# Kernel optimization log

Measured on AMD Instinct MI355X. Metric: run time of the kernel, lower is better.

## Reference

```python
import jax, jax.numpy as jnp
import numpy as np

INPUT_SIZE = 64
HIDDEN = 256
OUTPUT_SIZE = 64
NUM_LAYERS = 2
MAX_LENGTH = 512
BATCH = 1024


def setup_inputs() -> dict:
    key = jax.random.key(0)
    ks = jax.random.split(key, 14)
    s = 1.0 / np.sqrt(HIDDEN)  # torch LSTM/Linear init scale
    f32 = jnp.float32
    inp = {
        "batch_size": BATCH,
        "h0": jax.random.normal(ks[0], (NUM_LAYERS, BATCH, HIDDEN), f32),
        "c0": jax.random.normal(ks[1], (NUM_LAYERS, BATCH, HIDDEN), f32),
        "Wih0": jax.random.uniform(ks[2], (4 * HIDDEN, INPUT_SIZE), f32, -s, s),
        "Whh0": jax.random.uniform(ks[3], (4 * HIDDEN, HIDDEN), f32, -s, s),
        "bih0": jax.random.uniform(ks[4], (4 * HIDDEN,), f32, -s, s),
        "bhh0": jax.random.uniform(ks[5], (4 * HIDDEN,), f32, -s, s),
        "Wih1": jax.random.uniform(ks[6], (4 * HIDDEN, HIDDEN), f32, -s, s),
        "Whh1": jax.random.uniform(ks[7], (4 * HIDDEN, HIDDEN), f32, -s, s),
        "bih1": jax.random.uniform(ks[8], (4 * HIDDEN,), f32, -s, s),
        "bhh1": jax.random.uniform(ks[9], (4 * HIDDEN,), f32, -s, s),
        "Wfc": jax.random.uniform(ks[10], (OUTPUT_SIZE, HIDDEN), f32, -s, s),
        "bfc": jax.random.uniform(ks[11], (OUTPUT_SIZE,), f32, -s, s),
    }
    return inp


def _lstm_cell(x, h, c, Wih, Whh, bih, bhh):
    # torch gate order: input, forget, cell(g), output
    gates = x @ Wih.T + h @ Whh.T + bih + bhh  # [B, 4H]
    i, f, g, o = jnp.split(gates, 4, axis=-1)
    c_new = jax.nn.sigmoid(f) * c + jax.nn.sigmoid(i) * jnp.tanh(g)
    h_new = jax.nn.sigmoid(o) * jnp.tanh(c_new)
    return h_new, c_new


def reference(batch_size, h0, c0, Wih0, Whh0, bih0, bhh0, Wih1, Whh1, bih1, bhh1, Wfc, bfc):
    # initial decoder input: zeros with the (-3)rd feature set to 1 (SOS token)
    x0 = jnp.zeros((batch_size, INPUT_SIZE), h0.dtype).at[:, -3].set(1.0)

    def step(carry, _):
        x, h, c = carry  # h, c: [num_layers, B, H]
        h0_new, c0_new = _lstm_cell(x, h[0], c[0], Wih0, Whh0, bih0, bhh0)
        h1_new, c1_new = _lstm_cell(h0_new, h[1], c[1], Wih1, Whh1, bih1, bhh1)
        pred = h1_new @ Wfc.T + bfc  # [B, output_size]
        acts = jax.nn.log_softmax(pred[:, : OUTPUT_SIZE - 1], axis=-1)
        dur = jax.nn.sigmoid(pred[:, OUTPUT_SIZE - 1 :])
        out = jnp.concatenate([acts, dur], axis=-1)
        h_new = jnp.stack([h0_new, h1_new])
        c_new = jnp.stack([c0_new, c1_new])
        return (out, h_new, c_new), out

    (x_f, h_f, c_f), outs = jax.lax.scan(step, (x0, h0, c0), None, length=MAX_LENGTH)
    outputs = jnp.transpose(outs, (1, 0, 2))  # [B, max_length, output_size]
    return outputs, h_f, c_f
```

## Files before the change

### kernel.cpp

```cpp
#include <hip/hip_runtime.h>
#include <stdint.h>
#include <stddef.h>


#define NGROUP 16
#define GWG    16
#define NTHR   512
#define TSTEPS 512

typedef _Float16 half8 __attribute__((ext_vector_type(8)));
typedef float    f32x4 __attribute__((ext_vector_type(4)));

#define OUT_ELEMS   33554432
#define HF_ELEMS    524288
#define HBUF_ELEMS  16384
#define GROUP_WS_BYTES 65536
#define WS_HBUF_OFF 4096
#define WS_NEEDED   (WS_HBUF_OFF + NGROUP * GROUP_WS_BYTES)

__device__ __forceinline__ float sigm(float x)   { return 1.0f / (1.0f + __expf(-x)); }
__device__ __forceinline__ float tanh_f(float x) { return 1.0f - 2.0f / (__expf(2.0f * x) + 1.0f); }

__device__ __forceinline__ void group_barrier(int* ctr, int* phase, int zz) {
  __syncthreads();
  if (threadIdx.x == 0) {
    __hip_atomic_fetch_add(ctr, 1, __ATOMIC_RELEASE, __HIP_MEMORY_SCOPE_WORKGROUP);
    const int target = GWG * (++(*phase));
    while (__hip_atomic_fetch_add(ctr, zz, __ATOMIC_RELAXED, __HIP_MEMORY_SCOPE_WORKGROUP) < target)
      __builtin_amdgcn_s_sleep(1);
    asm volatile("buffer_inv sc0" ::: "memory");
  }
  __syncthreads();
}

__device__ __forceinline__ half8 ld_frag(const _Float16* buf, int idx16) {
  return *(const half8*)(buf + (size_t)idx16 * 8);
}

__device__ __forceinline__ void stage32k8(const void* src, void* lds_dst, int tid) {
  const int wv = tid >> 6;
  const int ln = tid & 63;
  const char* s = (const char*)src + ln * 16;
  char* d = (char*)lds_dst;
  #pragma unroll
  for (int i = 0; i < 4; ++i) {
    const int off = (i * 8 + wv) * 1024;
    __builtin_amdgcn_global_load_lds(
        (const __attribute__((address_space(1))) void*)(s + off),
        (__attribute__((address_space(3))) void*)(d + off),
        16, 0, 0);
  }
}

__global__ __launch_bounds__(NTHR, 2)
void decoder_kernel(const float* __restrict__ h0in, const float* __restrict__ c0in,
                    const float* __restrict__ Wih0, const float* __restrict__ Whh0,
                    const float* __restrict__ bih0, const float* __restrict__ bhh0,
                    const float* __restrict__ Wih1, const float* __restrict__ Whh1,
                    const float* __restrict__ bih1, const float* __restrict__ bhh1,
                    const float* __restrict__ Wfc,  const float* __restrict__ bfc,
                    float* __restrict__ out, char* __restrict__ ws)
{
  const int tid  = threadIdx.x;
  const int lane = tid & 63;
  const int wave = tid >> 6;
  const int mi   = wave >> 2;
  const int nj   = wave & 3;
  const int q    = lane >> 4;
  const int u    = lane & 15;
  const int em   = tid >> 3;
  const int eu2  = (tid & 7) * 2;

  int zz;
  asm volatile("s_mov_b32 %0, 0" : "=s"(zz));

  __shared__ int s_gw[2];
  if (tid == 0) {
    uint32_t xcc;
    asm volatile("s_getreg_b32 %0, hwreg(HW_REG_XCC_ID)" : "=s"(xcc));
    xcc &= 7;
    const int slot = atomicAdd((int*)(ws + 2048) + (size_t)xcc * 32, 1);
    s_gw[0] = (int)xcc * 2 + (slot >> 4);
    s_gw[1] = slot & 15;
  }
  __syncthreads();
  const int g = s_gw[0];
  const int w = s_gw[1];

  int* ctr = (int*)(ws + (size_t)g * 128);
  _Float16* h0b = (_Float16*)(ws + WS_HBUF_OFF + (size_t)g * GROUP_WS_BYTES);
  _Float16* h1b = h0b + HBUF_ELEMS;

  __shared__ __align__(16) _Float16 sb0[HBUF_ELEMS];
  __shared__ __align__(16) _Float16 sb1[HBUF_ELEMS];
  __shared__ __align__(16) _Float16 wfcs[32 * 65 * 8];
  __shared__ __align__(16) _Float16 xbuf[64 * 72];
  __shared__ __align__(16) float    exch[4 * 64 * 17];
  __shared__ __align__(16) float    predbuf[64 * 68];

  half8 bL0[10]; half8 bL1[16];
  float biasL0, biasL1, biasFC;
  {
    const int row = nj * 256 + w * 16 + u;
    biasL0 = bih0[row] + bhh0[row];
    biasL1 = bih1[row] + bhh1[row];
    #pragma unroll
    for (int kt = 0; kt < 10; ++kt) {
      const int k0 = kt * 32 + q * 8;
      const float* src = (kt < 2) ? (Wih0 + (size_t)row * 64 + k0)
                                  : (Whh0 + (size_t)row * 256 + (k0 - 64));
      half8 v;
      #pragma unroll
      for (int j = 0; j < 8; ++j) v[j] = (_Float16)src[j];
      bL0[kt] = v;
    }
    #pragma unroll
    for (int kt = 0; kt < 16; ++kt) {
      const int k0 = kt * 32 + q * 8;
      const float* src = (kt < 8) ? (Wih1 + (size_t)row * 256 + k0)
                                  : (Whh1 + (size_t)row * 256 + (k0 - 256));
      half8 v;
      #pragma unroll
      for (int j = 0; j < 8; ++j) v[j] = (_Float16)src[j];
      bL1[kt] = v;
    }
    biasFC = bfc[nj * 16 + u];
  }
  for (int i = tid; i < 2048; i += NTHR) {
    const int rowF = i & 63;
    const int c    = i >> 6;
    const float* s = Wfc + (size_t)rowF * 256 + c * 8;
    half8 v;
    #pragma unroll
    for (int j = 0; j < 8; ++j) v[j] = (_Float16)s[j];
    *(half8*)(wfcs + (size_t)(c * 65 + rowF) * 8) = v;
  }

  float c0st[2], c1st[2], h0sv[2], h1sv[2];
  #pragma unroll
  for (int e = 0; e < 2; ++e) {
    const size_t idx = (size_t)(g * 64 + em) * 256 + w * 16 + eu2 + e;
    c0st[e] = c0in[idx];
    c1st[e] = c0in[262144 + idx];
    h0sv[e] = 0.0f; h1sv[e] = 0.0f;
  }
  {
    const int cg2 = w * 2 + (eu2 >> 3);
    const uint32_t slot = (uint32_t)(cg2 * 64 + em) * 4 + ((eu2 & 7) >> 1);
    #pragma unroll
    for (int l = 0; l < 2; ++l) {
      const float* s = h0in + (size_t)l * 262144 + (size_t)(g * 64 + em) * 256 + w * 16 + eu2;
      union { _Float16 h[2]; uint32_t u32; } pk;
      pk.h[0] = (_Float16)s[0]; pk.h[1] = (_Float16)s[1];
      ((uint32_t*)(l ? h1b : h0b))[slot] = pk.u32;
    }
  }
  for (int i = tid; i < 64 * 64; i += NTHR) {
    const int row = i >> 6, col = i & 63;
    xbuf[row * 72 + col] = (col == 61) ? (_Float16)1.0f : (_Float16)0.0f;
  }

  int phase = 0;
  group_barrier(ctr, &phase, zz);

  stage32k8(h0b, sb0, tid);
  stage32k8(h1b, sb1, tid);
  __syncthreads();

  for (int t = 0; t < TSTEPS; ++t) {
    {
      f32x4 acc[2];
      #pragma unroll
      for (int mt = 0; mt < 2; ++mt) {
        f32x4 v; v[0] = biasL0; v[1] = biasL0; v[2] = biasL0; v[3] = biasL0;
        acc[mt] = v;
      }
      #pragma unroll
      for (int kt = 0; kt < 10; ++kt) {
        half8 a[2];
        #pragma unroll
        for (int mt = 0; mt < 2; ++mt) {
          const int m = mi * 32 + mt * 16 + u;
          if (kt < 2) a[mt] = *(const half8*)(xbuf + m * 72 + kt * 32 + q * 8);
          else        a[mt] = *(const half8*)(sb0 + (size_t)((kt * 4 - 8 + q) * 64 + m) * 8);
        }
        #pragma unroll
        for (int mt = 0; mt < 2; ++mt)
          acc[mt] = __builtin_amdgcn_mfma_f32_16x16x32_f16(a[mt], bL0[kt], acc[mt], 0, 0, 0);
      }
      #pragma unroll
      for (int mt = 0; mt < 2; ++mt)
        #pragma unroll
        for (int r = 0; r < 4; ++r)
          exch[(nj * 64 + mi * 32 + mt * 16 + q * 4 + r) * 17 + u] = acc[mt][r];
    }
    __syncthreads();
    {
      float hv[2];
      #pragma unroll
      for (int e = 0; e < 2; ++e) {
        const int ec = eu2 + e;
        const float iv = exch[(0 * 64 + em) * 17 + ec];
        const float fv = exch[(1 * 64 + em) * 17 + ec];
        const float gv = exch[(2 * 64 + em) * 17 + ec];
        const float ov = exch[(3 * 64 + em) * 17 + ec];
        const float cn = sigm(fv) * c0st[e] + sigm(iv) * tanh_f(gv);
        c0st[e] = cn;
        const float hh = sigm(ov) * tanh_f(cn);
        h0sv[e] = hh; hv[e] = hh;
      }
      union { _Float16 h[2]; uint32_t u32; } pk;
      pk.h[0] = (_Float16)hv[0]; pk.h[1] = (_Float16)hv[1];
      ((uint32_t*)h0b)[(uint32_t)((w * 2 + (eu2 >> 3)) * 64 + em) * 4 + ((eu2 & 7) >> 1)] = pk.u32;
    }
    group_barrier(ctr, &phase, zz);

    stage32k8(h0b, sb0, tid);

    {
      f32x4 acc[2];
      #pragma unroll
      for (int mt = 0; mt < 2; ++mt) {
        f32x4 v; v[0] = biasL1; v[1] = biasL1; v[2] = biasL1; v[3] = biasL1;
        acc[mt] = v;
      }
      #pragma unroll
      for (int kt = 8; kt < 16; ++kt) {
        half8 a[2];
        #pragma unroll
        for (int mt = 0; mt < 2; ++mt) {
          const int m = mi * 32 + mt * 16 + u;
          a[mt] = *(const half8*)(sb1 + (size_t)(((kt - 8) * 4 + q) * 64 + m) * 8);
        }
        #pragma unroll
        for (int mt = 0; mt < 2; ++mt)
          acc[mt] = __builtin_amdgcn_mfma_f32_16x16x32_f16(a[mt], bL1[kt], acc[mt], 0, 0, 0);
      }
      __syncthreads();
      #pragma unroll
      for (int kt = 0; kt < 8; ++kt) {
        half8 a[2];
        #pragma unroll
        for (int mt = 0; mt < 2; ++mt) {
          const int m = mi * 32 + mt * 16 + u;
          a[mt] = *(const half8*)(sb0 + (size_t)((kt * 4 + q) * 64 + m) * 8);
        }
        #pragma unroll
        for (int mt = 0; mt < 2; ++mt)
          acc[mt] = __builtin_amdgcn_mfma_f32_16x16x32_f16(a[mt], bL1[kt], acc[mt], 0, 0, 0);
      }
      #pragma unroll
      for (int mt = 0; mt < 2; ++mt)
        #pragma unroll
        for (int r = 0; r < 4; ++r)
          exch[(nj * 64 + mi * 32 + mt * 16 + q * 4 + r) * 17 + u] = acc[mt][r];
    }
    __syncthreads();
    {
      float hv[2];
      #pragma unroll
      for (int e = 0; e < 2; ++e) {
        const int ec = eu2 + e;
        const float iv = exch[(0 * 64 + em) * 17 + ec];
        const float fv = exch[(1 * 64 + em) * 17 + ec];
        const float gv = exch[(2 * 64 + em) * 17 + ec];
        const float ov = exch[(3 * 64 + em) * 17 + ec];
        const float cn = sigm(fv) * c1st[e] + sigm(iv) * tanh_f(gv);
        c1st[e] = cn;
        const float hh = sigm(ov) * tanh_f(cn);
        h1sv[e] = hh; hv[e] = hh;
      }
      union { _Float16 h[2]; uint32_t u32; } pk;
      pk.h[0] = (_Float16)hv[0]; pk.h[1] = (_Float16)hv[1];
      ((uint32_t*)h1b)[(uint32_t)((w * 2 + (eu2 >> 3)) * 64 + em) * 4 + ((eu2 & 7) >> 1)] = pk.u32;
    }
    group_barrier(ctr, &phase, zz);

    stage32k8(h1b, sb1, tid);

    {
      f32x4 accF[2];
      #pragma unroll
      for (int mt = 0; mt < 2; ++mt) {
        f32x4 v; v[0] = biasFC; v[1] = biasFC; v[2] = biasFC; v[3] = biasFC;
        accF[mt] = v;
      }
      #pragma unroll
      for (int kt = 0; kt < 8; ++kt) {
        const half8 b = *(const half8*)(wfcs + (size_t)((kt * 4 + q) * 65 + nj * 16 + u) * 8);
        half8 a[2];
        #pragma unroll
        for (int mt = 0; mt < 2; ++mt)
          a[mt] = ld_frag(h1b, (kt * 4 + q) * 64 + (mi * 32 + mt * 16 + u));
        #pragma unroll
        for (int mt = 0; mt < 2; ++mt)
          accF[mt] = __builtin_amdgcn_mfma_f32_16x16x32_f16(a[mt], b, accF[mt], 0, 0, 0);
      }
      #pragma unroll
      for (int mt = 0; mt < 2; ++mt)
        #pragma unroll
        for (int r = 0; r < 4; ++r)
          predbuf[(mi * 32 + mt * 16 + q * 4 + r) * 68 + nj * 16 + u] = accF[mt][r];
    }
    __syncthreads();
    {
      const int row = tid >> 3;
      const int cg  = tid & 7;
      const float* pr = predbuf + row * 68 + cg * 8;
      float p[8];
      #pragma unroll
      for (int j = 0; j < 8; ++j) p[j] = pr[j];
      float mx = -3.0e38f;
      #pragma unroll
      for (int j = 0; j < 8; ++j)
        if (!(cg == 7 && j == 7)) mx = fmaxf(mx, p[j]);
      mx = fmaxf(mx, __shfl_xor(mx, 1));
      mx = fmaxf(mx, __shfl_xor(mx, 2));
      mx = fmaxf(mx, __shfl_xor(mx, 4));
      float sm = 0.0f;
      #pragma unroll
      for (int j = 0; j < 8; ++j)
        if (!(cg == 7 && j == 7)) sm += __expf(p[j] - mx);
      sm += __shfl_xor(sm, 1);
      sm += __shfl_xor(sm, 2);
      sm += __shfl_xor(sm, 4);
      const float lz = mx + __logf(sm);
      float o[8];
      #pragma unroll
      for (int j = 0; j < 8; ++j) o[j] = p[j] - lz;
      if (cg == 7) o[7] = sigm(p[7]);
      _Float16* xw = xbuf + row * 72 + cg * 8;
      #pragma unroll
      for (int j = 0; j < 8; ++j) xw[j] = (_Float16)o[j];
      if ((row >> 2) == w) {
        const int ch = g * 64 + row;
        float* dst = out + ((size_t)ch * TSTEPS + t) * 64 + cg * 8;
        #pragma unroll
        for (int j = 0; j < 8; ++j) dst[j] = o[j];
      }
    }
    __syncthreads();
  }

  {
    float* hfp = out + OUT_ELEMS;
    float* cfp = out + OUT_ELEMS + HF_ELEMS;
    #pragma unroll
    for (int e = 0; e < 2; ++e) {
      const size_t idx = (size_t)(g * 64 + em) * 256 + w * 16 + eu2 + e;
      hfp[idx]          = h0sv[e];
      hfp[262144 + idx] = h1sv[e];
      cfp[idx]          = c0st[e];
      cfp[262144 + idx] = c1st[e];
    }
  }
}

extern "C" void kernel_launch(void* const* d_in, const int* in_sizes, int n_in,
                              void* d_out, int out_size, void* d_ws, size_t ws_size,
                              hipStream_t stream) {
  (void)in_sizes; (void)n_in; (void)out_size;
  if (ws_size < (size_t)WS_NEEDED) return;

  const float* h0   = (const float*)d_in[1];
  const float* c0   = (const float*)d_in[2];
  const float* Wih0 = (const float*)d_in[3];
  const float* Whh0 = (const float*)d_in[4];
  const float* bih0 = (const float*)d_in[5];
  const float* bhh0 = (const float*)d_in[6];
  const float* Wih1 = (const float*)d_in[7];
  const float* Whh1 = (const float*)d_in[8];
  const float* bih1 = (const float*)d_in[9];
  const float* bhh1 = (const float*)d_in[10];
  const float* Wfc  = (const float*)d_in[11];
  const float* bfc  = (const float*)d_in[12];
  float* outp = (float*)d_out;
  char*  wsp  = (char*)d_ws;

  hipMemsetAsync(d_ws, 0, WS_HBUF_OFF, stream);

  void* args[] = { &h0, &c0, &Wih0, &Whh0, &bih0, &bhh0, &Wih1, &Whh1,
                   &bih1, &bhh1, &Wfc, &bfc, &outp, &wsp };
  hipError_t e = hipLaunchCooperativeKernel((const void*)decoder_kernel,
                                            dim3(NGROUP * GWG), dim3(NTHR),
                                            args, 0u, stream);
  if (e != hipSuccess) {
    decoder_kernel<<<dim3(NGROUP * GWG), dim3(NTHR), 0, stream>>>(
        h0, c0, Wih0, Whh0, bih0, bhh0, Wih1, Whh1, bih1, bhh1, Wfc, bfc, outp, wsp);
  }
}
```

Before: 3.340 ms.

## Split batch into 32 groups of 32 rows to double workgroup count

```diff
diff --git a/kernel.cpp b/kernel.cpp
--- a/kernel.cpp
+++ b/kernel.cpp
@@ -3,7 +3,7 @@
 #include <stddef.h>
 
 
-#define NGROUP 16
+#define NGROUP 32
 #define GWG    16
 #define NTHR   512
 #define TSTEPS 512
@@ -13,9 +13,10 @@
 
 #define OUT_ELEMS   33554432
 #define HF_ELEMS    524288
-#define HBUF_ELEMS  16384
-#define GROUP_WS_BYTES 65536
-#define WS_HBUF_OFF 4096
+#define HBUF_ELEMS  8192
+#define GROUP_WS_BYTES 32768
+#define WS_SLOT_OFF 4096
+#define WS_HBUF_OFF 8192
 #define WS_NEEDED   (WS_HBUF_OFF + NGROUP * GROUP_WS_BYTES)
 
 __device__ __forceinline__ float sigm(float x)   { return 1.0f / (1.0f + __expf(-x)); }
@@ -37,13 +38,13 @@
   return *(const half8*)(buf + (size_t)idx16 * 8);
 }
 
-__device__ __forceinline__ void stage32k8(const void* src, void* lds_dst, int tid) {
+__device__ __forceinline__ void stage16k8(const void* src, void* lds_dst, int tid) {
   const int wv = tid >> 6;
   const int ln = tid & 63;
   const char* s = (const char*)src + ln * 16;
   char* d = (char*)lds_dst;
   #pragma unroll
-  for (int i = 0; i < 4; ++i) {
+  for (int i = 0; i < 2; ++i) {
     const int off = (i * 8 + wv) * 1024;
     __builtin_amdgcn_global_load_lds(
         (const __attribute__((address_space(1))) void*)(s + off),
@@ -52,7 +53,7 @@
   }
 }
 
-__global__ __launch_bounds__(NTHR, 2)
+__global__ __launch_bounds__(NTHR, 4)
 void decoder_kernel(const float* __restrict__ h0in, const float* __restrict__ c0in,
                     const float* __restrict__ Wih0, const float* __restrict__ Whh0,
                     const float* __restrict__ bih0, const float* __restrict__ bhh0,
@@ -68,8 +69,8 @@
   const int nj   = wave & 3;
   const int q    = lane >> 4;
   const int u    = lane & 15;
-  const int em   = tid >> 3;
-  const int eu2  = (tid & 7) * 2;
+  const int em   = tid >> 4;
+  const int eu   = tid & 15;
 
   int zz;
   asm volatile("s_mov_b32 %0, 0" : "=s"(zz));
@@ -79,8 +80,8 @@
     uint32_t xcc;
     asm volatile("s_getreg_b32 %0, hwreg(HW_REG_XCC_ID)" : "=s"(xcc));
     xcc &= 7;
-    const int slot = atomicAdd((int*)(ws + 2048) + (size_t)xcc * 32, 1);
-    s_gw[0] = (int)xcc * 2 + (slot >> 4);
+    const int slot = atomicAdd((int*)(ws + WS_SLOT_OFF) + (size_t)xcc * 32, 1);
+    s_gw[0] = (int)xcc * 4 + (slot >> 4);
     s_gw[1] = slot & 15;
   }
   __syncthreads();
@@ -94,9 +95,10 @@
   __shared__ __align__(16) _Float16 sb0[HBUF_ELEMS];
   __shared__ __align__(16) _Float16 sb1[HBUF_ELEMS];
   __shared__ __align__(16) _Float16 wfcs[32 * 65 * 8];
-  __shared__ __align__(16) _Float16 xbuf[64 * 72];
-  __shared__ __align__(16) float    exch[4 * 64 * 17];
-  __shared__ __align__(16) float    predbuf[64 * 68];
+  __shared__ __align__(16) _Float16 xbuf[32 * 72];
+  __shared__ __align__(16) float    xpbuf[2176];
+  float* exch    = xpbuf;
+  float* predbuf = xpbuf;
 
   half8 bL0[10]; half8 bL1[16];
   float biasL0, biasL1, biasFC;
@@ -136,26 +138,26 @@
     *(half8*)(wfcs + (size_t)(c * 65 + rowF) * 8) = v;
   }
 
-  float c0st[2], c1st[2], h0sv[2], h1sv[2];
-  #pragma unroll
-  for (int e = 0; e < 2; ++e) {
-    const size_t idx = (size_t)(g * 64 + em) * 256 + w * 16 + eu2 + e;
-    c0st[e] = c0in[idx];
-    c1st[e] = c0in[262144 + idx];
-    h0sv[e] = 0.0f; h1sv[e] = 0.0f;
-  }
+  float c0st, c1st, h0sv = 0.0f, h1sv = 0.0f;
   {
-    const int cg2 = w * 2 + (eu2 >> 3);
-    const uint32_t slot = (uint32_t)(cg2 * 64 + em) * 4 + ((eu2 & 7) >> 1);
+    const size_t idx = (size_t)(g * 32 + em) * 256 + w * 16 + eu;
+    c0st = c0in[idx];
+    c1st = c0in[262144 + idx];
+  }
+  if (tid < 64) {
+    const int m  = tid & 31;
+    const int cc = tid >> 5;
+    const int c  = w * 2 + cc;
     #pragma unroll
     for (int l = 0; l < 2; ++l) {
-      const float* s = h0in + (size_t)l * 262144 + (size_t)(g * 64 + em) * 256 + w * 16 + eu2;
-      union { _Float16 h[2]; uint32_t u32; } pk;
-      pk.h[0] = (_Float16)s[0]; pk.h[1] = (_Float16)s[1];
-      ((uint32_t*)(l ? h1b : h0b))[slot] = pk.u32;
-    }
-  }
-  for (int i = tid; i < 64 * 64; i += NTHR) {
+      const float* s = h0in + (size_t)l * 262144 + (size_t)(g * 32 + m) * 256 + c * 8;
+      half8 pk;
+      #pragma unroll
+      for (int j = 0; j < 8; ++j) pk[j] = (_Float16)s[j];
+      *(half8*)((l ? h1b : h0b) + (size_t)(c * 32 + m) * 8) = pk;
+    }
+  }
+  for (int i = tid; i < 32 * 64; i += NTHR) {
     const int row = i >> 6, col = i & 63;
     xbuf[row * 72 + col] = (col == 61) ? (_Float16)1.0f : (_Float16)0.0f;
   }
@@ -163,180 +165,138 @@
   int phase = 0;
   group_barrier(ctr, &phase, zz);
 
-  stage32k8(h0b, sb0, tid);
-  stage32k8(h1b, sb1, tid);
+  stage16k8(h0b, sb0, tid);
+  stage16k8(h1b, sb1, tid);
   __syncthreads();
 
   for (int t = 0; t < TSTEPS; ++t) {
     {
-      f32x4 acc[2];
-      #pragma unroll
-      for (int mt = 0; mt < 2; ++mt) {
-        f32x4 v; v[0] = biasL0; v[1] = biasL0; v[2] = biasL0; v[3] = biasL0;
-        acc[mt] = v;
-      }
+      f32x4 acc;
+      acc[0] = biasL0; acc[1] = biasL0; acc[2] = biasL0; acc[3] = biasL0;
+      const int m_ = mi * 16 + u;
       #pragma unroll
       for (int kt = 0; kt < 10; ++kt) {
-        half8 a[2];
-        #pragma unroll
-        for (int mt = 0; mt < 2; ++mt) {
-          const int m = mi * 32 + mt * 16 + u;
-          if (kt < 2) a[mt] = *(const half8*)(xbuf + m * 72 + kt * 32 + q * 8);
-          else        a[mt] = *(const half8*)(sb0 + (size_t)((kt * 4 - 8 + q) * 64 + m) * 8);
-        }
-        #pragma unroll
-        for (int mt = 0; mt < 2; ++mt)
-          acc[mt] = __builtin_amdgcn_mfma_f32_16x16x32_f16(a[mt], bL0[kt], acc[mt], 0, 0, 0);
-      }
-      #pragma unroll
-      for (int mt = 0; mt < 2; ++mt)
-        #pragma unroll
-        for (int r = 0; r < 4; ++r)
-          exch[(nj * 64 + mi * 32 + mt * 16 + q * 4 + r) * 17 + u] = acc[mt][r];
+        half8 a;
+        if (kt < 2) a = *(const half8*)(xbuf + m_ * 72 + kt * 32 + q * 8);
+        else        a = *(const half8*)(sb0 + (size_t)((kt * 4 - 8 + q) * 32 + m_) * 8);
+        acc = __builtin_amdgcn_mfma_f32_16x16x32_f16(a, bL0[kt], acc, 0, 0, 0);
+      }
+      #pragma unroll
+      for (int r = 0; r < 4; ++r)
+        exch[(nj * 32 + mi * 16 + q * 4 + r) * 17 + u] = acc[r];
     }
     __syncthreads();
     {
-      float hv[2];
-      #pragma unroll
-      for (int e = 0; e < 2; ++e) {
-        const int ec = eu2 + e;
-        const float iv = exch[(0 * 64 + em) * 17 + ec];
-        const float fv = exch[(1 * 64 + em) * 17 + ec];
-        const float gv = exch[(2 * 64 + em) * 17 + ec];
-        const float ov = exch[(3 * 64 + em) * 17 + ec];
-        const float cn = sigm(fv) * c0st[e] + sigm(iv) * tanh_f(gv);
-        c0st[e] = cn;
-        const float hh = sigm(ov) * tanh_f(cn);
-        h0sv[e] = hh; hv[e] = hh;
-      }
-      union { _Float16 h[2]; uint32_t u32; } pk;
-      pk.h[0] = (_Float16)hv[0]; pk.h[1] = (_Float16)hv[1];
-      ((uint32_t*)h0b)[(uint32_t)((w * 2 + (eu2 >> 3)) * 64 + em) * 4 + ((eu2 & 7) >> 1)] = pk.u32;
+      const float iv = exch[(0 * 32 + em) * 17 + eu];
+      const float fv = exch[(1 * 32 + em) * 17 + eu];
+      const float gv = exch[(2 * 32 + em) * 17 + eu];
+      const float ov = exch[(3 * 32 + em) * 17 + eu];
+      const float cn = sigm(fv) * c0st + sigm(iv) * tanh_f(gv);
+      c0st = cn;
+      const float hh = sigm(ov) * tanh_f(cn);
+      h0sv = hh;
+      const float other = __shfl_xor(hh, 1);
+      if (!(eu & 1)) {
+        union { _Float16 h[2]; uint32_t u32; } pk;
+        pk.h[0] = (_Float16)hh; pk.h[1] = (_Float16)other;
+        ((uint32_t*)h0b)[(uint32_t)((w * 2 + (eu >> 3)) * 32 + em) * 4 + ((eu & 7) >> 1)] = pk.u32;
+      }
     }
     group_barrier(ctr, &phase, zz);
 
-    stage32k8(h0b, sb0, tid);
-
-    {
-      f32x4 acc[2];
-      #pragma unroll
-      for (int mt = 0; mt < 2; ++mt) {
-        f32x4 v; v[0] = biasL1; v[1] = biasL1; v[2] = biasL1; v[3] = biasL1;
-        acc[mt] = v;
-      }
+    stage16k8(h0b, sb0, tid);
+
+    {
+      f32x4 acc;
+      acc[0] = biasL1; acc[1] = biasL1; acc[2] = biasL1; acc[3] = biasL1;
+      const int m_ = mi * 16 + u;
       #pragma unroll
       for (int kt = 8; kt < 16; ++kt) {
-        half8 a[2];
-        #pragma unroll
-        for (int mt = 0; mt < 2; ++mt) {
-          const int m = mi * 32 + mt * 16 + u;
-          a[mt] = *(const half8*)(sb1 + (size_t)(((kt - 8) * 4 + q) * 64 + m) * 8);
-        }
-        #pragma unroll
-        for (int mt = 0; mt < 2; ++mt)
-          acc[mt] = __builtin_amdgcn_mfma_f32_16x16x32_f16(a[mt], bL1[kt], acc[mt], 0, 0, 0);
+        const half8 a = *(const half8*)(sb1 + (size_t)(((kt - 8) * 4 + q) * 32 + m_) * 8);
+        acc = __builtin_amdgcn_mfma_f32_16x16x32_f16(a, bL1[kt], acc, 0, 0, 0);
       }
       __syncthreads();
       #pragma unroll
       for (int kt = 0; kt < 8; ++kt) {
-        half8 a[2];
-        #pragma unroll
-        for (int mt = 0; mt < 2; ++mt) {
-          const int m = mi * 32 + mt * 16 + u;
-          a[mt] = *(const half8*)(sb0 + (size_t)((kt * 4 + q) * 64 + m) * 8);
-        }
-        #pragma unroll
-        for (int mt = 0; mt < 2; ++mt)
-          acc[mt] = __builtin_amdgcn_mfma_f32_16x16x32_f16(a[mt], bL1[kt], acc[mt], 0, 0, 0);
-      }
-      #pragma unroll
-      for (int mt = 0; mt < 2; ++mt)
-        #pragma unroll
-        for (int r = 0; r < 4; ++r)
-          exch[(nj * 64 + mi * 32 + mt * 16 + q * 4 + r) * 17 + u] = acc[mt][r];
+        const half8 a = *(const half8*)(sb0 + (size_t)((kt * 4 + q) * 32 + m_) * 8);
+        acc = __builtin_amdgcn_mfma_f32_16x16x32_f16(a, bL1[kt], acc, 0, 0, 0);
+      }
+      #pragma unroll
+      for (int r = 0; r < 4; ++r)
+        exch[(nj * 32 + mi * 16 + q * 4 + r) * 17 + u] = acc[r];
     }
     __syncthreads();
     {
-      float hv[2];
-      #pragma unroll
-      for (int e = 0; e < 2; ++e) {
-        const int ec = eu2 + e;
-        const float iv = exch[(0 * 64 + em) * 17 + ec];
-        const float fv = exch[(1 * 64 + em) * 17 + ec];
-        const float gv = exch[(2 * 64 + em) * 17 + ec];
-        const float ov = exch[(3 * 64 + em) * 17 + ec];
-        const float cn = sigm(fv) * c1st[e] + sigm(iv) * tanh_f(gv);
-        c1st[e] = cn;
-        const float hh = sigm(ov) * tanh_f(cn);
-        h1sv[e] = hh; hv[e] = hh;
-      }
-      union { _Float16 h[2]; uint32_t u32; } pk;
-      pk.h[0] = (_Float16)hv[0]; pk.h[1] = (_Float16)hv[1];
-      ((uint32_t*)h1b)[(uint32_t)((w * 2 + (eu2 >> 3)) * 64 + em) * 4 + ((eu2 & 7) >> 1)] = pk.u32;
+      const float iv = exch[(0 * 32 + em) * 17 + eu];
+      const float fv = exch[(1 * 32 + em) * 17 + eu];
+      const float gv = exch[(2 * 32 + em) * 17 + eu];
+      const float ov = exch[(3 * 32 + em) * 17 + eu];
+      const float cn = sigm(fv) * c1st + sigm(iv) * tanh_f(gv);
+      c1st = cn;
+      const float hh = sigm(ov) * tanh_f(cn);
+      h1sv = hh;
+      const float other = __shfl_xor(hh, 1);
+      if (!(eu & 1)) {
+        union { _Float16 h[2]; uint32_t u32; } pk;
+        pk.h[0] = (_Float16)hh; pk.h[1] = (_Float16)other;
+        ((uint32_t*)h1b)[(uint32_t)((w * 2 + (eu >> 3)) * 32 + em) * 4 + ((eu & 7) >> 1)] = pk.u32;
+      }
     }
     group_barrier(ctr, &phase, zz);
 
-    stage32k8(h1b, sb1, tid);
-
-    {
-      f32x4 accF[2];
-      #pragma unroll
-      for (int mt = 0; mt < 2; ++mt) {
-        f32x4 v; v[0] = biasFC; v[1] = biasFC; v[2] = biasFC; v[3] = biasFC;
-        accF[mt] = v;
-      }
+    stage16k8(h1b, sb1, tid);
+
+    {
+      f32x4 accF;
+      accF[0] = biasFC; accF[1] = biasFC; accF[2] = biasFC; accF[3] = biasFC;
+      const int m_ = mi * 16 + u;
       #pragma unroll
       for (int kt = 0; kt < 8; ++kt) {
         const half8 b = *(const half8*)(wfcs + (size_t)((kt * 4 + q) * 65 + nj * 16 + u) * 8);
-        half8 a[2];
-        #pragma unroll
-        for (int mt = 0; mt < 2; ++mt)
-          a[mt] = ld_frag(h1b, (kt * 4 + q) * 64 + (mi * 32 + mt * 16 + u));
-        #pragma unroll
-        for (int mt = 0; mt < 2; ++mt)
-          accF[mt] = __builtin_amdgcn_mfma_f32_16x16x32_f16(a[mt], b, accF[mt], 0, 0, 0);
-      }
-      #pragma unroll
-      for (int mt = 0; mt < 2; ++mt)
-        #pragma unroll
-        for (int r = 0; r < 4; ++r)
-          predbuf[(mi * 32 + mt * 16 + q * 4 + r) * 68 + nj * 16 + u] = accF[mt][r];
+        const half8 a = ld_frag(h1b, (kt * 4 + q) * 32 + m_);
+        accF = __builtin_amdgcn_mfma_f32_16x16x32_f16(a, b, accF, 0, 0, 0);
+      }
+      #pragma unroll
+      for (int r = 0; r < 4; ++r)
+        predbuf[(mi * 16 + q * 4 + r) * 65 + nj * 16 + u] = accF[r];
     }
     __syncthreads();
     {
-      const int row = tid >> 3;
-      const int cg  = tid & 7;
-      const float* pr = predbuf + row * 68 + cg * 8;
-      float p[8];
-      #pragma unroll
-      for (int j = 0; j < 8; ++j) p[j] = pr[j];
+      const int row = tid >> 4;
+      const int cg  = tid & 15;
+      const float* pr = predbuf + row * 65 + cg * 4;
+      float p[4];
+      #pragma unroll
+      for (int j = 0; j < 4; ++j) p[j] = pr[j];
       float mx = -3.0e38f;
       #pragma unroll
-      for (int j = 0; j < 8; ++j)
-        if (!(cg == 7 && j == 7)) mx = fmaxf(mx, p[j]);
+      for (int j = 0; j < 4; ++j)
+        if (!(cg == 15 && j == 3)) mx = fmaxf(mx, p[j]);
       mx = fmaxf(mx, __shfl_xor(mx, 1));
       mx = fmaxf(mx, __shfl_xor(mx, 2));
       mx = fmaxf(mx, __shfl_xor(mx, 4));
+      mx = fmaxf(mx, __shfl_xor(mx, 8));
       float sm = 0.0f;
       #pragma unroll
-      for (int j = 0; j < 8; ++j)
-        if (!(cg == 7 && j == 7)) sm += __expf(p[j] - mx);
+      for (int j = 0; j < 4; ++j)
+        if (!(cg == 15 && j == 3)) sm += __expf(p[j] - mx);
       sm += __shfl_xor(sm, 1);
       sm += __shfl_xor(sm, 2);
       sm += __shfl_xor(sm, 4);
+      sm += __shfl_xor(sm, 8);
       const float lz = mx + __logf(sm);
-      float o[8];
-      #pragma unroll
-      for (int j = 0; j < 8; ++j) o[j] = p[j] - lz;
-      if (cg == 7) o[7] = sigm(p[7]);
-      _Float16* xw = xbuf + row * 72 + cg * 8;
-      #pragma unroll
-      for (int j = 0; j < 8; ++j) xw[j] = (_Float16)o[j];
-      if ((row >> 2) == w) {
-        const int ch = g * 64 + row;
-        float* dst = out + ((size_t)ch * TSTEPS + t) * 64 + cg * 8;
+      float o[4];
+      #pragma unroll
+      for (int j = 0; j < 4; ++j) o[j] = p[j] - lz;
+      if (cg == 15) o[3] = sigm(p[3]);
+      _Float16* xw = xbuf + row * 72 + cg * 4;
+      #pragma unroll
+      for (int j = 0; j < 4; ++j) xw[j] = (_Float16)o[j];
+      if ((row >> 1) == w) {
+        const int ch = g * 32 + row;
+        float* dst = out + ((size_t)ch * TSTEPS + t) * 64 + cg * 4;
         #pragma unroll
-        for (int j = 0; j < 8; ++j) dst[j] = o[j];
+        for (int j = 0; j < 4; ++j) dst[j] = o[j];
       }
     }
     __syncthreads();
@@ -345,14 +305,11 @@
   {
     float* hfp = out + OUT_ELEMS;
     float* cfp = out + OUT_ELEMS + HF_ELEMS;
-    #pragma unroll
-    for (int e = 0; e < 2; ++e) {
-      const size_t idx = (size_t)(g * 64 + em) * 256 + w * 16 + eu2 + e;
-      hfp[idx]          = h0sv[e];
-      hfp[262144 + idx] = h1sv[e];
-      cfp[idx]          = c0st[e];
-      cfp[262144 + idx] = c1st[e];
-    }
+    const size_t idx = (size_t)(g * 32 + em) * 256 + w * 16 + eu;
+    hfp[idx]          = h0sv;
+    hfp[262144 + idx] = h1sv;
+    cfp[idx]          = c0st;
+    cfp[262144 + idx] = c1st;
   }
 }
 
```

New measurement: 7.661 ms. +129.4%, slower.

## Split each workgroup into two independent 32-row virtual blocks with wave-level barriers

Applied to the files above, without the earlier changes.

```diff
diff --git a/kernel.cpp b/kernel.cpp
--- a/kernel.cpp
+++ b/kernel.cpp
@@ -3,9 +3,10 @@
 #include <stddef.h>
 
 
-#define NGROUP 16
-#define GWG    16
+#define NGROUP 32
+#define VBWG   16
 #define NTHR   512
+#define NBLK   256
 #define TSTEPS 512
 
 typedef _Float16 half8 __attribute__((ext_vector_type(8)));
@@ -13,38 +14,57 @@
 
 #define OUT_ELEMS   33554432
 #define HF_ELEMS    524288
-#define HBUF_ELEMS  16384
-#define GROUP_WS_BYTES 65536
-#define WS_HBUF_OFF 4096
+#define HBUF_ELEMS  8192
+#define GROUP_WS_BYTES 32768
+#define WS_SLOT_OFF 4096
+#define WS_HBUF_OFF 8192
 #define WS_NEEDED   (WS_HBUF_OFF + NGROUP * GROUP_WS_BYTES)
 
 __device__ __forceinline__ float sigm(float x)   { return 1.0f / (1.0f + __expf(-x)); }
 __device__ __forceinline__ float tanh_f(float x) { return 1.0f - 2.0f / (__expf(2.0f * x) + 1.0f); }
 
-__device__ __forceinline__ void group_barrier(int* ctr, int* phase, int zz) {
-  __syncthreads();
-  if (threadIdx.x == 0) {
+__device__ __forceinline__ void vb_bar(int* vbctr, int* vbph, int lane) {
+  asm volatile("s_waitcnt vmcnt(0) lgkmcnt(0)" ::: "memory");
+  const int target = 4 * (++(*vbph));
+  if (lane == 0) {
+    __hip_atomic_fetch_add(vbctr, 1, __ATOMIC_RELEASE, __HIP_MEMORY_SCOPE_WORKGROUP);
+    while (__hip_atomic_load(vbctr, __ATOMIC_RELAXED, __HIP_MEMORY_SCOPE_WORKGROUP) < target)
+      __builtin_amdgcn_s_sleep(1);
+  }
+  asm volatile("s_waitcnt lgkmcnt(0)" ::: "memory");
+}
+
+__device__ __forceinline__ void group_bar(int* ctr, int* gph, int zz,
+                                          int* vbctr, int* vbph, int* vbdone,
+                                          int wv, int lane) {
+  vb_bar(vbctr, vbph, lane);
+  const int ep = ++(*gph);
+  if (wv == 0 && lane == 0) {
     __hip_atomic_fetch_add(ctr, 1, __ATOMIC_RELEASE, __HIP_MEMORY_SCOPE_WORKGROUP);
-    const int target = GWG * (++(*phase));
+    const int target = VBWG * ep;
     while (__hip_atomic_fetch_add(ctr, zz, __ATOMIC_RELAXED, __HIP_MEMORY_SCOPE_WORKGROUP) < target)
       __builtin_amdgcn_s_sleep(1);
     asm volatile("buffer_inv sc0" ::: "memory");
-  }
-  __syncthreads();
+    __hip_atomic_store(vbdone, ep, __ATOMIC_RELEASE, __HIP_MEMORY_SCOPE_WORKGROUP);
+  }
+  if (lane == 0) {
+    while (__hip_atomic_load(vbdone, __ATOMIC_RELAXED, __HIP_MEMORY_SCOPE_WORKGROUP) < ep)
+      __builtin_amdgcn_s_sleep(1);
+  }
+  asm volatile("s_waitcnt lgkmcnt(0)" ::: "memory");
 }
 
 __device__ __forceinline__ half8 ld_frag(const _Float16* buf, int idx16) {
   return *(const half8*)(buf + (size_t)idx16 * 8);
 }
 
-__device__ __forceinline__ void stage32k8(const void* src, void* lds_dst, int tid) {
-  const int wv = tid >> 6;
-  const int ln = tid & 63;
-  const char* s = (const char*)src + ln * 16;
+__device__ __forceinline__ void stage16k4(const void* src, void* lds_dst,
+                                          int wv, int lane) {
+  const char* s = (const char*)src + lane * 16;
   char* d = (char*)lds_dst;
   #pragma unroll
   for (int i = 0; i < 4; ++i) {
-    const int off = (i * 8 + wv) * 1024;
+    const int off = (i * 4 + wv) * 1024;
     __builtin_amdgcn_global_load_lds(
         (const __attribute__((address_space(1))) void*)(s + off),
         (__attribute__((address_space(3))) void*)(d + off),
@@ -63,40 +83,45 @@
 {
   const int tid  = threadIdx.x;
   const int lane = tid & 63;
-  const int wave = tid >> 6;
-  const int mi   = wave >> 2;
-  const int nj   = wave & 3;
+  const int vb   = tid >> 8;
+  const int vtid = tid & 255;
+  const int wv   = vtid >> 6;
+  const int nj   = wv;
   const int q    = lane >> 4;
   const int u    = lane & 15;
-  const int em   = tid >> 3;
-  const int eu2  = (tid & 7) * 2;
+  const int em   = vtid >> 3;
+  const int eu2  = (vtid & 7) * 2;
 
   int zz;
   asm volatile("s_mov_b32 %0, 0" : "=s"(zz));
 
   __shared__ int s_gw[2];
+  __shared__ int vbctr[2], vbdone[2];
   if (tid == 0) {
     uint32_t xcc;
     asm volatile("s_getreg_b32 %0, hwreg(HW_REG_XCC_ID)" : "=s"(xcc));
     xcc &= 7;
-    const int slot = atomicAdd((int*)(ws + 2048) + (size_t)xcc * 32, 1);
-    s_gw[0] = (int)xcc * 2 + (slot >> 4);
+    const int slot = atomicAdd((int*)(ws + WS_SLOT_OFF) + (size_t)xcc * 32, 1);
+    s_gw[0] = (int)xcc * 4 + (slot >> 4) * 2;
     s_gw[1] = slot & 15;
   }
+  if (tid < 2) { vbctr[tid] = 0; vbdone[tid] = 0; }
   __syncthreads();
-  const int g = s_gw[0];
+  const int g = s_gw[0] + vb;
   const int w = s_gw[1];
 
   int* ctr = (int*)(ws + (size_t)g * 128);
   _Float16* h0b = (_Float16*)(ws + WS_HBUF_OFF + (size_t)g * GROUP_WS_BYTES);
   _Float16* h1b = h0b + HBUF_ELEMS;
 
-  __shared__ __align__(16) _Float16 sb0[HBUF_ELEMS];
-  __shared__ __align__(16) _Float16 sb1[HBUF_ELEMS];
+  __shared__ __align__(16) _Float16 sb0[2][HBUF_ELEMS];
+  __shared__ __align__(16) _Float16 sb1[2][HBUF_ELEMS];
   __shared__ __align__(16) _Float16 wfcs[32 * 65 * 8];
-  __shared__ __align__(16) _Float16 xbuf[64 * 72];
-  __shared__ __align__(16) float    exch[4 * 64 * 17];
-  __shared__ __align__(16) float    predbuf[64 * 68];
+  __shared__ __align__(16) _Float16 xbuf[2][32 * 72];
+  __shared__ __align__(16) float    xpbuf[2][2176];
+
+  float* exch    = xpbuf[vb];
+  float* predbuf = xpbuf[vb];
 
   half8 bL0[10]; half8 bL1[16];
   float biasL0, biasL1, biasFC;
@@ -139,33 +164,38 @@
   float c0st[2], c1st[2], h0sv[2], h1sv[2];
   #pragma unroll
   for (int e = 0; e < 2; ++e) {
-    const size_t idx = (size_t)(g * 64 + em) * 256 + w * 16 + eu2 + e;
+    const size_t idx = (size_t)(g * 32 + em) * 256 + w * 16 + eu2 + e;
     c0st[e] = c0in[idx];
     c1st[e] = c0in[262144 + idx];
     h0sv[e] = 0.0f; h1sv[e] = 0.0f;
   }
-  {
-    const int cg2 = w * 2 + (eu2 >> 3);
-    const uint32_t slot = (uint32_t)(cg2 * 64 + em) * 4 + ((eu2 & 7) >> 1);
+  if (vtid < 64) {
+    const int m  = vtid & 31;
+    const int cc = vtid >> 5;
+    const int c  = w * 2 + cc;
     #pragma unroll
     for (int l = 0; l < 2; ++l) {
-      const float* s = h0in + (size_t)l * 262144 + (size_t)(g * 64 + em) * 256 + w * 16 + eu2;
-      union { _Float16 h[2]; uint32_t u32; } pk;
-      pk.h[0] = (_Float16)s[0]; pk.h[1] = (_Float16)s[1];
-      ((uint32_t*)(l ? h1b : h0b))[slot] = pk.u32;
-    }
-  }
-  for (int i = tid; i < 64 * 64; i += NTHR) {
+      const float* s = h0in + (size_t)l * 262144 + (size_t)(g * 32 + m) * 256 + c * 8;
+      half8 pk;
+      #pragma unroll
+      for (int j = 0; j < 8; ++j) pk[j] = (_Float16)s[j];
+      *(half8*)((l ? h1b : h0b) + (size_t)(c * 32 + m) * 8) = pk;
+    }
+  }
+  for (int i = vtid; i < 32 * 64; i += 256) {
     const int row = i >> 6, col = i & 63;
-    xbuf[row * 72 + col] = (col == 61) ? (_Float16)1.0f : (_Float16)0.0f;
-  }
-
-  int phase = 0;
-  group_barrier(ctr, &phase, zz);
-
-  stage32k8(h0b, sb0, tid);
-  stage32k8(h1b, sb1, tid);
+    xbuf[vb][row * 72 + col] = (col == 61) ? (_Float16)1.0f : (_Float16)0.0f;
+  }
+
+  int vbph = 0, gph = 0;
+  int* myctr  = &vbctr[vb];
+  int* mydone = &vbdone[vb];
   __syncthreads();
+  group_bar(ctr, &gph, zz, myctr, &vbph, mydone, wv, lane);
+
+  stage16k4(h0b, sb0[vb], wv, lane);
+  stage16k4(h1b, sb1[vb], wv, lane);
+  vb_bar(myctr, &vbph, lane);
 
   for (int t = 0; t < TSTEPS; ++t) {
     {
@@ -177,33 +207,31 @@
       }
       #pragma unroll
       for (int kt = 0; kt < 10; ++kt) {
-        half8 a[2];
         #pragma unroll
         for (int mt = 0; mt < 2; ++mt) {
-          const int m = mi * 32 + mt * 16 + u;
-          if (kt < 2) a[mt] = *(const half8*)(xbuf + m * 72 + kt * 32 + q * 8);
-          else        a[mt] = *(const half8*)(sb0 + (size_t)((kt * 4 - 8 + q) * 64 + m) * 8);
+          const int m = mt * 16 + u;
+          half8 a;
+          if (kt < 2) a = *(const half8*)(xbuf[vb] + m * 72 + kt * 32 + q * 8);
+          else        a = *(const half8*)(sb0[vb] + (size_t)((kt * 4 - 8 + q) * 32 + m) * 8);
+          acc[mt] = __builtin_amdgcn_mfma_f32_16x16x32_f16(a, bL0[kt], acc[mt], 0, 0, 0);
         }
-        #pragma unroll
-        for (int mt = 0; mt < 2; ++mt)
-          acc[mt] = __builtin_amdgcn_mfma_f32_16x16x32_f16(a[mt], bL0[kt], acc[mt], 0, 0, 0);
       }
       #pragma unroll
       for (int mt = 0; mt < 2; ++mt)
         #pragma unroll
         for (int r = 0; r < 4; ++r)
-          exch[(nj * 64 + mi * 32 + mt * 16 + q * 4 + r) * 17 + u] = acc[mt][r];
-    }
-    __syncthreads();
+          exch[(nj * 32 + mt * 16 + q * 4 + r) * 17 + u] = acc[mt][r];
+    }
+    vb_bar(myctr, &vbph, lane);
     {
       float hv[2];
       #pragma unroll
       for (int e = 0; e < 2; ++e) {
         const int ec = eu2 + e;
-        const float iv = exch[(0 * 64 + em) * 17 + ec];
-        const float fv = exch[(1 * 64 + em) * 17 + ec];
-        const float gv = exch[(2 * 64 + em) * 17 + ec];
-        const float ov = exch[(3 * 64 + em) * 17 + ec];
+        const float iv = exch[(0 * 32 + em) * 17 + ec];
+        const float fv = exch[(1 * 32 + em) * 17 + ec];
+        const float gv = exch[(2 * 32 + em) * 17 + ec];
+        const float ov = exch[(3 * 32 + em) * 17 + ec];
         const float cn = sigm(fv) * c0st[e] + sigm(iv) * tanh_f(gv);
         c0st[e] = cn;
         const float hh = sigm(ov) * tanh_f(cn);
@@ -211,11 +239,11 @@
       }
       union { _Float16 h[2]; uint32_t u32; } pk;
       pk.h[0] = (_Float16)hv[0]; pk.h[1] = (_Float16)hv[1];
-      ((uint32_t*)h0b)[(uint32_t)((w * 2 + (eu2 >> 3)) * 64 + em) * 4 + ((eu2 & 7) >> 1)] = pk.u32;
-    }
-    group_barrier(ctr, &phase, zz);
-
-    stage32k8(h0b, sb0, tid);
+      ((uint32_t*)h0b)[(uint32_t)((w * 2 + (eu2 >> 3)) * 32 + em) * 4 + ((eu2 & 7) >> 1)] = pk.u32;
+    }
+    group_bar(ctr, &gph, zz, myctr, &vbph, mydone, wv, lane);
+
+    stage16k4(h0b, sb0[vb], wv, lane);
 
     {
       f32x4 acc[2];
@@ -226,45 +254,39 @@
       }
       #pragma unroll
       for (int kt = 8; kt < 16; ++kt) {
-        half8 a[2];
         #pragma unroll
         for (int mt = 0; mt < 2; ++mt) {
-          const int m = mi * 32 + mt * 16 + u;
-          a[mt] = *(const half8*)(sb1 + (size_t)(((kt - 8) * 4 + q) * 64 + m) * 8);
+          const int m = mt * 16 + u;
+          const half8 a = *(const half8*)(sb1[vb] + (size_t)(((kt - 8) * 4 + q) * 32 + m) * 8);
+          acc[mt] = __builtin_amdgcn_mfma_f32_16x16x32_f16(a, bL1[kt], acc[mt], 0, 0, 0);
         }
-        #pragma unroll
-        for (int mt = 0; mt < 2; ++mt)
-          acc[mt] = __builtin_amdgcn_mfma_f32_16x16x32_f16(a[mt], bL1[kt], acc[mt], 0, 0, 0);
-      }
-      __syncthreads();
+      }
+      vb_bar(myctr, &vbph, lane);
       #pragma unroll
       for (int kt = 0; kt < 8; ++kt) {
-        half8 a[2];
         #pragma unroll
         for (int mt = 0; mt < 2; ++mt) {
-          const int m = mi * 32 + mt * 16 + u;
-          a[mt] = *(const half8*)(sb0 + (size_t)((kt * 4 + q) * 64 + m) * 8);
+          const int m = mt * 16 + u;
+          const half8 a = *(const half8*)(sb0[vb] + (size_t)((kt * 4 + q) * 32 + m) * 8);
+          acc[mt] = __builtin_amdgcn_mfma_f32_16x16x32_f16(a, bL1[kt], acc[mt], 0, 0, 0);
         }
-        #pragma unroll
-        for (int mt = 0; mt < 2; ++mt)
-          acc[mt] = __builtin_amdgcn_mfma_f32_16x16x32_f16(a[mt], bL1[kt], acc[mt], 0, 0, 0);
       }
       #pragma unroll
       for (int mt = 0; mt < 2; ++mt)
         #pragma unroll
         for (int r = 0; r < 4; ++r)
-          exch[(nj * 64 + mi * 32 + mt * 16 + q * 4 + r) * 17 + u] = acc[mt][r];
-    }
-    __syncthreads();
+          exch[(nj * 32 + mt * 16 + q * 4 + r) * 17 + u] = acc[mt][r];
+    }
+    vb_bar(myctr, &vbph, lane);
     {
       float hv[2];
       #pragma unroll
       for (int e = 0; e < 2; ++e) {
         const int ec = eu2 + e;
-        const float iv = exch[(0 * 64 + em) * 17 + ec];
-        const float fv = exch[(1 * 64 + em) * 17 + ec];
-        const float gv = exch[(2 * 64 + em) * 17 + ec];
-        const float ov = exch[(3 * 64 + em) * 17 + ec];
+        const float iv = exch[(0 * 32 + em) * 17 + ec];
+        const float fv = exch[(1 * 32 + em) * 17 + ec];
+        const float gv = exch[(2 * 32 + em) * 17 + ec];
+        const float ov = exch[(3 * 32 + em) * 17 + ec];
         const float cn = sigm(fv) * c1st[e] + sigm(iv) * tanh_f(gv);
         c1st[e] = cn;
         const float hh = sigm(ov) * tanh_f(cn);
@@ -272,11 +294,11 @@
       }
       union { _Float16 h[2]; uint32_t u32; } pk;
       pk.h[0] = (_Float16)hv[0]; pk.h[1] = (_Float16)hv[1];
-      ((uint32_t*)h1b)[(uint32_t)((w * 2 + (eu2 >> 3)) * 64 + em) * 4 + ((eu2 & 7) >> 1)] = pk.u32;
-    }
-    group_barrier(ctr, &phase, zz);
-
-    stage32k8(h1b, sb1, tid);
+      ((uint32_t*)h1b)[(uint32_t)((w * 2 + (eu2 >> 3)) * 32 + em) * 4 + ((eu2 & 7) >> 1)] = pk.u32;
+    }
+    group_bar(ctr, &gph, zz, myctr, &vbph, mydone, wv, lane);
+
+    stage16k4(h1b, sb1[vb], wv, lane);
 
     {
       f32x4 accF[2];
@@ -288,25 +310,23 @@
       #pragma unroll
       for (int kt = 0; kt < 8; ++kt) {
         const half8 b = *(const half8*)(wfcs + (size_t)((kt * 4 + q) * 65 + nj * 16 + u) * 8);
-        half8 a[2];
-        #pragma unroll
-        for (int mt = 0; mt < 2; ++mt)
-          a[mt] = ld_frag(h1b, (kt * 4 + q) * 64 + (mi * 32 + mt * 16 + u));
-        #pragma unroll
-        for (int mt = 0; mt < 2; ++mt)
-          accF[mt] = __builtin_amdgcn_mfma_f32_16x16x32_f16(a[mt], b, accF[mt], 0, 0, 0);
+        #pragma unroll
+        for (int mt = 0; mt < 2; ++mt) {
+          const half8 a = ld_frag(h1b, (kt * 4 + q) * 32 + mt * 16 + u);
+          accF[mt] = __builtin_amdgcn_mfma_f32_16x16x32_f16(a, b, accF[mt], 0, 0, 0);
+        }
       }
       #pragma unroll
       for (int mt = 0; mt < 2; ++mt)
         #pragma unroll
         for (int r = 0; r < 4; ++r)
-          predbuf[(mi * 32 + mt * 16 + q * 4 + r) * 68 + nj * 16 + u] = accF[mt][r];
-    }
-    __syncthreads();
-    {
-      const int row = tid >> 3;
-      const int cg  = tid & 7;
-      const float* pr = predbuf + row * 68 + cg * 8;
+          predbuf[(mt * 16 + q * 4 + r) * 65 + nj * 16 + u] = accF[mt][r];
+    }
+    vb_bar(myctr, &vbph, lane);
+    {
+      const int row = vtid >> 3;
+      const int cg  = vtid & 7;
+      const float* pr = predbuf + row * 65 + cg * 8;
       float p[8];
       #pragma unroll
       for (int j = 0; j < 8; ++j) p[j] = pr[j];
@@ -329,17 +349,17 @@
       #pragma unroll
       for (int j = 0; j < 8; ++j) o[j] = p[j] - lz;
       if (cg == 7) o[7] = sigm(p[7]);
-      _Float16* xw = xbuf + row * 72 + cg * 8;
+      _Float16* xw = xbuf[vb] + row * 72 + cg * 8;
       #pragma unroll
       for (int j = 0; j < 8; ++j) xw[j] = (_Float16)o[j];
-      if ((row >> 2) == w) {
-        const int ch = g * 64 + row;
+      if ((row >> 1) == w) {
+        const int ch = g * 32 + row;
         float* dst = out + ((size_t)ch * TSTEPS + t) * 64 + cg * 8;
         #pragma unroll
         for (int j = 0; j < 8; ++j) dst[j] = o[j];
       }
     }
-    __syncthreads();
+    vb_bar(myctr, &vbph, lane);
   }
 
   {
@@ -347,7 +367,7 @@
     float* cfp = out + OUT_ELEMS + HF_ELEMS;
     #pragma unroll
     for (int e = 0; e < 2; ++e) {
-      const size_t idx = (size_t)(g * 64 + em) * 256 + w * 16 + eu2 + e;
+      const size_t idx = (size_t)(g * 32 + em) * 256 + w * 16 + eu2 + e;
       hfp[idx]          = h0sv[e];
       hfp[262144 + idx] = h1sv[e];
       cfp[idx]          = c0st[e];
@@ -382,10 +402,10 @@
   void* args[] = { &h0, &c0, &Wih0, &Whh0, &bih0, &bhh0, &Wih1, &Whh1,
                    &bih1, &bhh1, &Wfc, &bfc, &outp, &wsp };
   hipError_t e = hipLaunchCooperativeKernel((const void*)decoder_kernel,
-                                            dim3(NGROUP * GWG), dim3(NTHR),
+                                            dim3(NBLK), dim3(NTHR),
                                             args, 0u, stream);
   if (e != hipSuccess) {
-    decoder_kernel<<<dim3(NGROUP * GWG), dim3(NTHR), 0, stream>>>(
+    decoder_kernel<<<dim3(NBLK), dim3(NTHR), 0, stream>>>(
         h0, c0, Wih0, Whh0, bih0, bhh0, Wih1, Whh1, bih1, bhh1, Wfc, bfc, outp, wsp);
   }
 }
```

Measured after the change: 3.512 ms. 1.05x slower.
